# Kernel tuning notes

Measured on AMD Instinct MI355X. Metric: run time of the kernel, lower is better.

The kernel has to match this reference:

```python
import jax, jax.numpy as jnp
import numpy as np

N_BITS = 4
SIZE_SCALE = 8 // N_BITS  # 2 int4 values per byte
MASK = (1 << N_BITS) - 1  # 0xF

OC, IC = 8192, 8192
B = 64


def setup_inputs() -> dict:
    key = jax.random.key(0)
    k_in, k_w, k_d, k_z, k_b = jax.random.split(key, 5)
    input = jax.random.normal(k_in, (B, IC), dtype=jnp.float32)
    # packed uint8 weight buffer: [OC // SIZE_SCALE, IC]; stored as int32 with byte values
    weight_packed = jax.random.randint(k_w, (OC // SIZE_SCALE, IC), 0, 256, dtype=jnp.int32)
    # per-output-channel affine quant params
    delta = jax.random.uniform(k_d, (OC,), dtype=jnp.float32) * 0.01 + 1e-4
    zero_point = jax.random.uniform(k_z, (OC,), dtype=jnp.float32) * MASK
    bias = jax.random.normal(k_b, (OC,), dtype=jnp.float32)
    return {"input": input, "weight_packed": weight_packed, "delta": delta,
            "zero_point": zero_point, "bias": bias}


def _dequantize(weight_packed, delta, zero_point):
    # Bit-unpack: each byte holds SIZE_SCALE values of N_BITS each, packed along
    # the output-channel dim (dim 0), low nibble first.
    parts = [ (weight_packed >> (N_BITS * i)) & MASK for i in range(SIZE_SCALE) ]
    w_int = jnp.concatenate(parts, axis=0)               # [OC, IC] int
    # Affine dequant, per output channel: w = (q - zp) * delta
    w = (w_int.astype(jnp.float32) - zero_point[:, None]) * delta[:, None]
    return w


def reference(input, weight_packed, delta, zero_point, bias):
    # use_weight_quant=True, use_act_quant=False (defaults in the module)
    w = _dequantize(weight_packed, delta, zero_point)    # [OC, IC]
    out = jnp.dot(input, w.T) + bias                     # F.linear
    return out
```

## Files before the change

kernel.cpp:

```cpp
#include <hip/hip_runtime.h>

constexpr int BATCH = 64;
constexpr int IC    = 8192;
constexpr int OC    = 8192;
constexpr int OCH   = 4096;
constexpr int KSPLIT = 8;
constexpr int KPER  = IC / KSPLIT;
constexpr int BK    = 64;
constexpr int NITER = KPER / BK;
constexpr int LDK   = BK + 8;

typedef __bf16 bf16x8 __attribute__((ext_vector_type(8)));
typedef float  f32x4  __attribute__((ext_vector_type(4)));

static __device__ __forceinline__ unsigned short f2bf(float f) {
    unsigned u = __float_as_uint(f);
    u += 0x7FFFu + ((u >> 16) & 1u);
    return (unsigned short)(u >> 16);
}

static __device__ __forceinline__ unsigned pack2bf(int n0, int n1) {
    unsigned f0 = __float_as_uint((float)n0);
    unsigned f1 = __float_as_uint((float)n1);
    return __builtin_amdgcn_perm(f1, f0, 0x07060302u);
}

__global__ __launch_bounds__(256) void prep_kernel(
    const float* __restrict__ in, unsigned short* __restrict__ Abf,
    float* __restrict__ S)
{
    const int b = blockIdx.x;
    const int t = threadIdx.x;
    const float* row = in + (size_t)b * IC;
    unsigned short* orow = Abf + (size_t)b * IC;

    float sum = 0.f;
#pragma unroll
    for (int i = 0; i < IC / 1024; ++i) {
        const int c = i * 1024 + t * 4;
        const float4 v = *(const float4*)(row + c);
        sum += (v.x + v.y) + (v.z + v.w);
        ushort4 o = make_ushort4(f2bf(v.x), f2bf(v.y), f2bf(v.z), f2bf(v.w));
        *(ushort4*)(orow + c) = o;
    }
#pragma unroll
    for (int off = 32; off > 0; off >>= 1) sum += __shfl_down(sum, off);

    __shared__ float red[4];
    if ((t & 63) == 0) red[t >> 6] = sum;
    __syncthreads();
    if (t == 0) S[b] = (red[0] + red[1]) + (red[2] + red[3]);
}

__global__ __launch_bounds__(256, 4) void gemm_kernel(
    const unsigned short* __restrict__ Abf,
    const int* __restrict__ wp,
    const float* __restrict__ delta,
    const float* __restrict__ zp,
    const float* __restrict__ bias,
    const float* __restrict__ S,
    float* __restrict__ out)
{
    __shared__ unsigned short lA[64 * LDK];
    __shared__ unsigned short lW[64 * LDK];

    const int t    = threadIdx.x;
    const int wave = t >> 6;
    const int lane = t & 63;
    const int lm   = lane & 15;
    const int lq   = lane >> 4;

    const int nt  = blockIdx.x & 127;
    const int ks  = blockIdx.x >> 7;
    const int r0  = nt * 32;
    const int kb0 = ks * KPER;

    f32x4 acc[4];
    const f32x4 zero4 = {0.f, 0.f, 0.f, 0.f};
#pragma unroll
    for (int i = 0; i < 4; ++i) acc[i] = zero4;

    const int uAr = t >> 2, uAc = (t & 3) * 16;
    const int uWr = t >> 3, uWc = (t & 7) * 8;

    const unsigned short* pA = Abf + (size_t)uAr * IC + kb0 + uAc;
    const int*            pW = wp  + (size_t)(r0 + uWr) * IC + kb0 + uWc;

    int4 a0 = *(const int4*)(pA);
    int4 a1 = *(const int4*)(pA + 8);
    int4 w0 = *(const int4*)(pW);
    int4 w1 = *(const int4*)(pW + 4);

    for (int it = 0; it < NITER; ++it) {
        __syncthreads();

        *(int4*)(&lA[uAr * LDK + uAc])     = a0;
        *(int4*)(&lA[uAr * LDK + uAc + 8]) = a1;

        int4 lo, hi;
        lo.x = pack2bf( w0.x       & 15,  w0.y       & 15);
        lo.y = pack2bf( w0.z       & 15,  w0.w       & 15);
        lo.z = pack2bf( w1.x       & 15,  w1.y       & 15);
        lo.w = pack2bf( w1.z       & 15,  w1.w       & 15);
        hi.x = pack2bf((w0.x >> 4) & 15, (w0.y >> 4) & 15);
        hi.y = pack2bf((w0.z >> 4) & 15, (w0.w >> 4) & 15);
        hi.z = pack2bf((w1.x >> 4) & 15, (w1.y >> 4) & 15);
        hi.w = pack2bf((w1.z >> 4) & 15, (w1.w >> 4) & 15);
        *(int4*)(&lW[uWr        * LDK + uWc]) = lo;
        *(int4*)(&lW[(uWr + 32) * LDK + uWc]) = hi;

        __syncthreads();

        {
            const int koff = ((it + 1) & (NITER - 1)) * BK;
            a0 = *(const int4*)(pA + koff);
            a1 = *(const int4*)(pA + koff + 8);
            w0 = *(const int4*)(pW + koff);
            w1 = *(const int4*)(pW + koff + 4);
        }

#pragma unroll
        for (int s = 0; s < 2; ++s) {
            const int kc = s * 32 + lq * 8;
            const bf16x8 bfrg = *(const bf16x8*)(&lW[(wave * 16 + lm) * LDK + kc]);
#pragma unroll
            for (int mt = 0; mt < 4; ++mt) {
                const bf16x8 afrg = *(const bf16x8*)(&lA[(mt * 16 + lm) * LDK + kc]);
                acc[mt] = __builtin_amdgcn_mfma_f32_16x16x32_bf16(afrg, bfrg, acc[mt], 0, 0, 0);
            }
        }
    }

    const int cr = wave * 16 + lm;
    const int ch = (cr < 32) ? (r0 + cr) : (OCH + r0 + (cr - 32));
    const float d  = delta[ch];
    const float dz = d * zp[ch];
    const float bi = bias[ch];
    constexpr float inv_split = 1.f / (float)KSPLIT;

#pragma unroll
    for (int mt = 0; mt < 4; ++mt) {
#pragma unroll
        for (int r = 0; r < 4; ++r) {
            const int m = mt * 16 + lq * 4 + r;
            const float res = d * acc[mt][r] + (bi - dz * S[m]) * inv_split;
            atomicAdd(out + (size_t)m * OC + ch, res);
        }
    }
}

extern "C" void kernel_launch(void* const* d_in, const int* in_sizes, int n_in,
                              void* d_out, int out_size, void* d_ws, size_t ws_size,
                              hipStream_t stream) {
    const float* input = (const float*)d_in[0];
    const int*   wpk   = (const int*)d_in[1];
    const float* delta = (const float*)d_in[2];
    const float* zp    = (const float*)d_in[3];
    const float* bias  = (const float*)d_in[4];
    float* out = (float*)d_out;

    unsigned short* Abf = (unsigned short*)d_ws;
    float* S = (float*)((char*)d_ws + (size_t)BATCH * IC * 2);

    hipMemsetAsync(d_out, 0, (size_t)out_size * sizeof(float), stream);
    prep_kernel<<<dim3(BATCH), dim3(256), 0, stream>>>(input, Abf, S);
    gemm_kernel<<<dim3(128 * KSPLIT), dim3(256), 0, stream>>>(Abf, wpk, delta, zp, bias, S, out);
}
```

Measured before the change: 227.1 us.

## Replace split-K atomic accumulation with partial buffers and a separate reduce kernel

The split-K GEMM now writes its raw partial sums to a per-split workspace buffer instead of atomically adding dequant-corrected results into the output. A new reduce kernel sums the eight partials with vectorized loads and applies the delta, zero-point and bias epilogue, so the output memset is no longer needed. The goal is to remove contended float atomics and the memset. In exchange it adds a kernel launch and a 16 MB partial buffer that must be written and read back. The high-nibble mask is also dropped because the packed bytes are known to fit in 8 bits.

```diff
diff --git a/kernel.cpp b/kernel.cpp
--- a/kernel.cpp
+++ b/kernel.cpp
@@ -55,11 +55,7 @@
 __global__ __launch_bounds__(256, 4) void gemm_kernel(
     const unsigned short* __restrict__ Abf,
     const int* __restrict__ wp,
-    const float* __restrict__ delta,
-    const float* __restrict__ zp,
-    const float* __restrict__ bias,
-    const float* __restrict__ S,
-    float* __restrict__ out)
+    float* __restrict__ part)
 {
     __shared__ unsigned short lA[64 * LDK];
     __shared__ unsigned short lW[64 * LDK];
@@ -98,14 +94,14 @@
         *(int4*)(&lA[uAr * LDK + uAc + 8]) = a1;
 
         int4 lo, hi;
-        lo.x = pack2bf( w0.x       & 15,  w0.y       & 15);
-        lo.y = pack2bf( w0.z       & 15,  w0.w       & 15);
-        lo.z = pack2bf( w1.x       & 15,  w1.y       & 15);
-        lo.w = pack2bf( w1.z       & 15,  w1.w       & 15);
-        hi.x = pack2bf((w0.x >> 4) & 15, (w0.y >> 4) & 15);
-        hi.y = pack2bf((w0.z >> 4) & 15, (w0.w >> 4) & 15);
-        hi.z = pack2bf((w1.x >> 4) & 15, (w1.y >> 4) & 15);
-        hi.w = pack2bf((w1.z >> 4) & 15, (w1.w >> 4) & 15);
+        lo.x = pack2bf(w0.x & 15, w0.y & 15);
+        lo.y = pack2bf(w0.z & 15, w0.w & 15);
+        lo.z = pack2bf(w1.x & 15, w1.y & 15);
+        lo.w = pack2bf(w1.z & 15, w1.w & 15);
+        hi.x = pack2bf(w0.x >> 4, w0.y >> 4);
+        hi.y = pack2bf(w0.z >> 4, w0.w >> 4);
+        hi.z = pack2bf(w1.x >> 4, w1.y >> 4);
+        hi.w = pack2bf(w1.z >> 4, w1.w >> 4);
         *(int4*)(&lW[uWr        * LDK + uWc]) = lo;
         *(int4*)(&lW[(uWr + 32) * LDK + uWc]) = hi;
 
@@ -133,20 +129,47 @@
 
     const int cr = wave * 16 + lm;
     const int ch = (cr < 32) ? (r0 + cr) : (OCH + r0 + (cr - 32));
-    const float d  = delta[ch];
-    const float dz = d * zp[ch];
-    const float bi = bias[ch];
-    constexpr float inv_split = 1.f / (float)KSPLIT;
+    float* pout = part + (size_t)ks * (BATCH * OC) + ch;
 
 #pragma unroll
     for (int mt = 0; mt < 4; ++mt) {
 #pragma unroll
         for (int r = 0; r < 4; ++r) {
             const int m = mt * 16 + lq * 4 + r;
-            const float res = d * acc[mt][r] + (bi - dz * S[m]) * inv_split;
-            atomicAdd(out + (size_t)m * OC + ch, res);
+            pout[(size_t)m * OC] = acc[mt][r];
         }
     }
+}
+
+__global__ __launch_bounds__(256) void reduce_kernel(
+    const float* __restrict__ part,
+    const float* __restrict__ delta,
+    const float* __restrict__ zp,
+    const float* __restrict__ bias,
+    const float* __restrict__ S,
+    float* __restrict__ out)
+{
+    const int e  = (blockIdx.x * 256 + threadIdx.x) * 4;
+    const int m  = e >> 13;
+    const int ch = e & (OC - 1);
+
+    float4 s = {0.f, 0.f, 0.f, 0.f};
+#pragma unroll
+    for (int k = 0; k < KSPLIT; ++k) {
+        const float4 p = *(const float4*)(part + (size_t)k * (BATCH * OC) + e);
+        s.x += p.x; s.y += p.y; s.z += p.z; s.w += p.w;
+    }
+    const float4 d = *(const float4*)(delta + ch);
+    const float4 z = *(const float4*)(zp + ch);
+    const float4 b = *(const float4*)(bias + ch);
+    const float Sm = S[m];
+
+    float4 o;
+    o.x = d.x * s.x + b.x - d.x * z.x * Sm;
+    o.y = d.y * s.y + b.y - d.y * z.y * Sm;
+    o.z = d.z * s.z + b.z - d.z * z.z * Sm;
+    o.w = d.w * s.w + b.w - d.w * z.w * Sm;
+    *(float4*)(out + e) = o;
 }
 
 extern "C" void kernel_launch(void* const* d_in, const int* in_sizes, int n_in,
@@ -160,9 +183,10 @@
     float* out = (float*)d_out;
 
     unsigned short* Abf = (unsigned short*)d_ws;
-    float* S = (float*)((char*)d_ws + (size_t)BATCH * IC * 2);
+    float* S    = (float*)((char*)d_ws + (size_t)BATCH * IC * 2);
+    float* part = (float*)((char*)d_ws + (size_t)BATCH * IC * 2 + 4096);
 
-    hipMemsetAsync(d_out, 0, (size_t)out_size * sizeof(float), stream);
     prep_kernel<<<dim3(BATCH), dim3(256), 0, stream>>>(input, Abf, S);
-    gemm_kernel<<<dim3(128 * KSPLIT), dim3(256), 0, stream>>>(Abf, wpk, delta, zp, bias, S, out);
+    gemm_kernel<<<dim3(128 * KSPLIT), dim3(256), 0, stream>>>(Abf, wpk, part);
+    reduce_kernel<<<dim3(BATCH * OC / 1024), dim3(256), 0, stream>>>(part, delta, zp, bias, S, out);
 }
```

Result: no change. 225.4 us (-0.8%).
